# Kernel optimization log

Measured on AMD Instinct MI355X. Metric: run time of the kernel, lower is better.

The kernel has to match this reference:

```python
import jax, jax.numpy as jnp
import numpy as np

NEG = -1e10
EPS = 1e-5
H = 4  # num_heads


def layer_norm(y, g, b):
    m = jnp.mean(y, axis=-1, keepdims=True)
    v = jnp.mean((y - m) ** 2, axis=-1, keepdims=True)
    return (y - m) * jax.lax.rsqrt(v + EPS) * g + b


def setup_inputs() -> dict:
    key = jax.random.key(0)
    B, N, C = 16, 1024, 256
    ks = jax.random.split(key, 12)
    std = 0.1  # matches trunc_normal_(std=0.1) init
    inp = {
        "x": jax.random.normal(ks[0], (B, N, C), jnp.float32),
        "K": jax.random.normal(ks[1], (B, N, N), jnp.float32),
        "n1": jax.random.randint(ks[2], (B,), 8, 33),
        "n2": jax.random.randint(ks[3], (B,), 8, 33),
        "qkv_w": jax.random.normal(ks[4], (3 * C, C), jnp.float32) * std,
        "qkv_b": jnp.zeros((3 * C,), jnp.float32),
        "proj_w": jax.random.normal(ks[5], (C, C), jnp.float32) * std,
        "proj_b": jnp.zeros((C,), jnp.float32),
        "ln1_g": jnp.ones((C,), jnp.float32),
        "ln1_b": jnp.zeros((C,), jnp.float32),
        "ln2_g": jnp.ones((C,), jnp.float32),
        "ln2_b": jnp.zeros((C,), jnp.float32),
        "fc1_w": jax.random.normal(ks[6], (4 * C, C), jnp.float32) * std,
        "fc1_b": jnp.zeros((4 * C,), jnp.float32),
        "fc2_w": jax.random.normal(ks[7], (C, 4 * C), jnp.float32) * std,
        "fc2_b": jnp.zeros((C,), jnp.float32),
    }
    return inp


def reference(x, K, n1, n2, qkv_w, qkv_b, proj_w, proj_b,
              ln1_g, ln1_b, ln2_g, ln2_b, fc1_w, fc1_b, fc2_w, fc2_b):
    B, N, C = x.shape
    D = C // H
    scale = D ** -0.5

    # --- attention block ---
    h = layer_norm(x, ln1_g, ln1_b)
    qkv = (h @ qkv_w.T + qkv_b).reshape(B, N, 3, H, D)
    qkv = jnp.transpose(qkv, (2, 0, 3, 1, 4))  # [3,B,H,N,D]
    q, k, v = qkv[0], qkv[1], qkv[2]

    attn = jnp.einsum('bhnd,bhmd->bhnm', q, k) * scale  # [B,H,N,N]

    # per-sample dynamic block mask: rows>=n1*n2 fully masked; cols>=n1*n2 masked
    nrc = (n1 * n2)[:, None]                  # [B,1]
    invalid = jnp.arange(N)[None, :] >= nrc   # [B,N]
    mask = invalid[:, :, None] | invalid[:, None, :]  # [B,N,N]
    attn = jnp.where(mask[:, None], NEG, attn)
    attn = attn + K[:, None]                  # broadcast K over heads

    a = jax.nn.softmax(attn, axis=-1)
    o = jnp.einsum('bhnm,bhmd->bhnd', a, v)
    o = jnp.transpose(o, (0, 2, 1, 3)).reshape(B, N, C)
    x = x + (o @ proj_w.T + proj_b)

    # --- MLP block (exact GELU as torch nn.GELU) ---
    h2 = layer_norm(x, ln2_g, ln2_b)
    m = jax.nn.gelu(h2 @ fc1_w.T + fc1_b, approximate=False)
    m = m @ fc2_w.T + fc2_b
    return x + m
```

## Files before the change

kernel.cpp:

```cpp
#include <hip/hip_runtime.h>
#include <math.h>
#include <stdint.h>

constexpr int Bc = 16, Nn = 1024, Cc = 256, Hh = 4;
constexpr int Mrows = Bc * Nn;
constexpr float EPSV = 1e-5f;

typedef __attribute__((ext_vector_type(4))) float f32x4;
typedef __attribute__((ext_vector_type(8))) short bf16x8;

__device__ inline float wave_reduce_sum(float v) {
#pragma unroll
  for (int m = 32; m >= 1; m >>= 1) v += __shfl_xor(v, m);
  return v;
}

__device__ inline short f2bf(float f) {
  uint32_t u = __builtin_bit_cast(uint32_t, f);
  u = (u + 0x7fffu + ((u >> 16) & 1u)) >> 16;
  return (short)u;
}
__device__ inline float bf2f(short s) {
  uint32_t u = ((uint32_t)(uint16_t)s) << 16;
  return __builtin_bit_cast(float, u);
}

__device__ inline float fexp(float x) {
  return __builtin_amdgcn_exp2f(x * 1.4426950408889634f);
}

__device__ inline float gelu_fast(float x) {
  float x2 = x * x;
  float u = x * (0.7978845608028654f + 0.0356774081f * x2);
  float e = __builtin_amdgcn_exp2f(u * 2.8853900817779268f);
  return x * (1.f - __builtin_amdgcn_rcpf(e + 1.f));
}

#define GLDS(gptr, lptr)                                             \
  __builtin_amdgcn_global_load_lds(                                  \
      (const __attribute__((address_space(1))) void*)(gptr),         \
      (__attribute__((address_space(3))) void*)(lptr), 16, 0, 0)

__global__ __launch_bounds__(256)
void cvt_bf16(const float* __restrict__ src, short* __restrict__ dst, int n) {
  int i = (blockIdx.x * 256 + threadIdx.x) * 4;
  if (i >= n) return;
  float4 v = *(const float4*)(src + i);
  short4 o;
  o.x = f2bf(v.x); o.y = f2bf(v.y); o.z = f2bf(v.z); o.w = f2bf(v.w);
  *(short4*)(dst + i) = o;
}

__global__ __launch_bounds__(256)
void ln_kernel(const float* __restrict__ x, const float* __restrict__ g,
               const float* __restrict__ b, short* __restrict__ h) {
  int row = blockIdx.x * 4 + (threadIdx.x >> 6);
  int lane = threadIdx.x & 63;
  const float4* xr = (const float4*)(x + (size_t)row * Cc);
  float4 v = xr[lane];
  float s = v.x + v.y + v.z + v.w;
  float sq = v.x * v.x + v.y * v.y + v.z * v.z + v.w * v.w;
  s = wave_reduce_sum(s);
  sq = wave_reduce_sum(sq);
  float mean = s * (1.f / Cc);
  float var = sq * (1.f / Cc) - mean * mean;
  float inv = rsqrtf(var + EPSV);
  float4 gg = ((const float4*)g)[lane];
  float4 bb = ((const float4*)b)[lane];
  short4 o;
  o.x = f2bf((v.x - mean) * inv * gg.x + bb.x);
  o.y = f2bf((v.y - mean) * inv * gg.y + bb.y);
  o.z = f2bf((v.z - mean) * inv * gg.z + bb.z);
  o.w = f2bf((v.w - mean) * inv * gg.w + bb.w);
  *(short4*)(h + (size_t)row * Cc + lane * 4) = o;
}

__global__ __launch_bounds__(256)
void qkv_mfma(const short* __restrict__ A, const short* __restrict__ Bw,
              const float* __restrict__ bias, short* __restrict__ qkp,
              short* __restrict__ vtp) {
  __shared__ __align__(16) short As[128 * 64];
  __shared__ __align__(16) short Bs[128 * 64];
  int t = threadIdx.x;
  int w = t >> 6, lane = t & 63;
  int wm = w >> 1, wn = w & 1;
  int l16 = lane & 15, lhi = lane >> 4;
  int m0 = blockIdx.y * 128, n0 = blockIdx.x * 128;
  const bool vblk = (n0 >= 512);
  f32x4 acc[4][4] = {};

  for (int k0 = 0; k0 < 256; k0 += 64) {
    __syncthreads();
#pragma unroll
    for (int i = 0; i < 4; ++i) {
      int cc = i * 256 + t;
      int r = cc >> 3, sl = cc & 7, ssl = sl ^ (r & 7);
      GLDS(A + (size_t)(m0 + r) * 256 + k0 + ssl * 8, &As[cc * 8]);
      GLDS(Bw + (size_t)(n0 + r) * 256 + k0 + ssl * 8, &Bs[cc * 8]);
    }
    asm volatile("s_waitcnt vmcnt(0)" ::: "memory");
    __syncthreads();
    if (!vblk) {
#pragma unroll
      for (int ks = 0; ks < 2; ++ks) {
        bf16x8 af[4], bg[4];
#pragma unroll
        for (int mi = 0; mi < 4; ++mi) {
          int row = wm * 64 + mi * 16 + l16;
          af[mi] = *(const bf16x8*)&As[row * 64 + ((ks * 32 + lhi * 8) ^ ((row & 7) << 3))];
        }
#pragma unroll
        for (int ni = 0; ni < 4; ++ni) {
          int row = wn * 64 + ni * 16 + l16;
          bg[ni] = *(const bf16x8*)&Bs[row * 64 + ((ks * 32 + lhi * 8) ^ ((row & 7) << 3))];
        }
#pragma unroll
        for (int mi = 0; mi < 4; ++mi)
#pragma unroll
          for (int ni = 0; ni < 4; ++ni)
            acc[mi][ni] = __builtin_amdgcn_mfma_f32_16x16x32_bf16(
                af[mi], bg[ni], acc[mi][ni], 0, 0, 0);
      }
    } else {
#pragma unroll
      for (int ks = 0; ks < 2; ++ks) {
        bf16x8 af[4], bg[4];
#pragma unroll
        for (int mi = 0; mi < 4; ++mi) {
          int row = wm * 64 + mi * 16 + l16;
          af[mi] = *(const bf16x8*)&As[row * 64 + ((ks * 32 + lhi * 8) ^ ((row & 7) << 3))];
        }
#pragma unroll
        for (int ni = 0; ni < 4; ++ni) {
          int row = wn * 64 + ni * 16 + l16;
          bg[ni] = *(const bf16x8*)&Bs[row * 64 + ((ks * 32 + lhi * 8) ^ ((row & 7) << 3))];
        }
#pragma unroll
        for (int mi = 0; mi < 4; ++mi)
#pragma unroll
          for (int ni = 0; ni < 4; ++ni)
            acc[mi][ni] = __builtin_amdgcn_mfma_f32_16x16x32_bf16(
                bg[ni], af[mi], acc[mi][ni], 0, 0, 0);
      }
    }
  }

  if (!vblk) {
    const bool isq = (n0 < 256);
#pragma unroll
    for (int mi = 0; mi < 4; ++mi) {
      int mbase = m0 + wm * 64 + mi * 16 + lhi * 4;
#pragma unroll
      for (int ni = 0; ni < 4; ++ni) {
        int n = n0 + wn * 64 + ni * 16 + l16;
        int s = n >> 8, hh = (n >> 6) & 3, d = n & 63;
        float bv = bias[n];
#pragma unroll
        for (int r = 0; r < 4; ++r) {
          int m = mbase + r;
          int b = m >> 10, rw = m & 1023;
          float v = acc[mi][ni][r] + bv;
          if (isq) v *= 0.125f;
          qkp[(size_t)s * 4194304 + (((size_t)(b * 4 + hh)) * 1024 + rw) * 64 + d] = f2bf(v);
        }
      }
    }
  } else {
#pragma unroll
    for (int mi = 0; mi < 4; ++mi) {
#pragma unroll
      for (int ni = 0; ni < 4; ++ni) {
#pragma unroll
        for (int r = 0; r < 4; ++r) {
          int n = n0 + wn * 64 + ni * 16 + lhi * 4 + r;
          int hh = (n >> 6) & 3, d = n & 63;
          int m = m0 + wm * 64 + mi * 16 + l16;
          int b = m >> 10, rw = m & 1023;
          float v = acc[mi][ni][r] + bias[n];
          vtp[(((size_t)(b * 4 + hh)) * 64 + d) * 1024 + rw] = f2bf(v);
        }
      }
    }
  }
}

__global__ __launch_bounds__(256)
void vmean_kernel(const short* __restrict__ vt, short* __restrict__ vmb) {
  __shared__ float part[64][4];
  int bh = blockIdx.x;
  int d = threadIdx.x >> 2, seg = threadIdx.x & 3;
  const short* p = vt + (size_t)bh * 65536 + (size_t)d * 1024 + seg * 256;
  float s = 0.f;
  for (int i = 0; i < 256; i += 8) {
    bf16x8 v = *(const bf16x8*)(p + i);
#pragma unroll
    for (int j = 0; j < 8; ++j) s += bf2f(v[j]);
  }
  part[d][seg] = s;
  __syncthreads();
  if (threadIdx.x < 64) {
    int dd = threadIdx.x;
    float tot = part[dd][0] + part[dd][1] + part[dd][2] + part[dd][3];
    vmb[bh * 64 + dd] = f2bf(tot * (1.f / 1024.f));
  }
}

__global__ __launch_bounds__(256)
void fattn_mfma(const short* __restrict__ qpk, const short* __restrict__ kpk,
                const short* __restrict__ vt, const float* __restrict__ Kmat,
                const int* __restrict__ n1, const int* __restrict__ n2,
                const short* __restrict__ vmb, short* __restrict__ o) {
  int bh = blockIdx.y, b = bh >> 2, hh = bh & 3;
  int row0 = blockIdx.x * 64;
  int nc = n1[b] * n2[b];
  int t = threadIdx.x;
  __shared__ short vms[64];
  if (t < 64) vms[t] = vmb[bh * 64 + t];
  __syncthreads();
  if (row0 >= nc) {
    for (int idx = t; idx < 4096; idx += 256) {
      int r = idx >> 6, d = idx & 63;
      o[((size_t)(b * 1024 + row0 + r)) * 256 + hh * 64 + d] = vms[d];
    }
    return;
  }
  __shared__ __align__(16) short Ks[2][64 * 64];
  __shared__ __align__(16) short Vs[2][64 * 64];
  __shared__ __align__(16) short Ps[64 * 64];
  int w = t >> 6, lane = t & 63, l16 = lane & 15, lhi = lane >> 4;

  constexpr float LOG2E = 1.4426950408889634f;
  constexpr float MREF = 12.0f;

  const short* qb = qpk + (size_t)bh * 65536 + (size_t)(row0 + w * 16 + l16) * 64;
  bf16x8 qf0 = *(const bf16x8*)(qb + lhi * 8);
  bf16x8 qf1 = *(const bf16x8*)(qb + 32 + lhi * 8);

  f32x4 accO[4] = {};
  float lsum[4] = {};
  const float* Kb = Kmat + (size_t)b * 1048576 + (size_t)(row0 + w * 16) * 1024;

  float kvp[16];

#pragma unroll
  for (int i = 0; i < 2; ++i) {
    int cc = i * 256 + t;
    int r = cc >> 3, sl = cc & 7, ssl = sl ^ (r & 7);
    GLDS(kpk + (size_t)bh * 65536 + (size_t)(0 + r) * 64 + ssl * 8, &Ks[0][cc * 8]);
    GLDS(vt + (size_t)bh * 65536 + (size_t)r * 1024 + 0 + ssl * 8, &Vs[0][cc * 8]);
  }
#pragma unroll
  for (int ni = 0; ni < 4; ++ni)
#pragma unroll
    for (int r = 0; r < 4; ++r)
      kvp[ni * 4 + r] =
          (Kb[(size_t)(lhi * 4 + r) * 1024 + 0 + ni * 16 + l16] - MREF) * LOG2E;

  int cur = 0;
  for (int j0 = 0; j0 < nc; j0 += 64, cur ^= 1) {
    asm volatile("s_waitcnt vmcnt(0)" ::: "memory");
    __syncthreads();

    float kvc[16];
#pragma unroll
    for (int i = 0; i < 16; ++i) kvc[i] = kvp[i];
    int jn = j0 + 64;
    if (jn < nc) {
      int nxt = cur ^ 1;
#pragma unroll
      for (int i = 0; i < 2; ++i) {
        int cc = i * 256 + t;
        int r = cc >> 3, sl = cc & 7, ssl = sl ^ (r & 7);
        GLDS(kpk + (size_t)bh * 65536 + (size_t)(jn + r) * 64 + ssl * 8, &Ks[nxt][cc * 8]);
        GLDS(vt + (size_t)bh * 65536 + (size_t)r * 1024 + jn + ssl * 8, &Vs[nxt][cc * 8]);
      }
#pragma unroll
      for (int ni = 0; ni < 4; ++ni)
#pragma unroll
        for (int r = 0; r < 4; ++r)
          kvp[ni * 4 + r] =
              (Kb[(size_t)(lhi * 4 + r) * 1024 + jn + ni * 16 + l16] - MREF) * LOG2E;
    }

    f32x4 accS[4] = {};
#pragma unroll
    for (int ks = 0; ks < 2; ++ks) {
#pragma unroll
      for (int ni = 0; ni < 4; ++ni) {
        int row = ni * 16 + l16;
        bf16x8 kf = *(const bf16x8*)&Ks[cur][row * 64 + (((ks * 4 + lhi) ^ (row & 7)) << 3)];
        accS[ni] = __builtin_amdgcn_mfma_f32_16x16x32_bf16(
            ks ? qf1 : qf0, kf, accS[ni], 0, 0, 0);
      }
    }

#pragma unroll
    for (int ni = 0; ni < 4; ++ni) {
      bool valid = (j0 + ni * 16 + l16) < nc;
#pragma unroll
      for (int r = 0; r < 4; ++r) {
        float e = __builtin_amdgcn_exp2f(fmaf(accS[ni][r], LOG2E, kvc[ni * 4 + r]));
        e = valid ? e : 0.f;
        lsum[r] += e;
        int prow = w * 16 + lhi * 4 + r;
        int col = ni * 16 + l16;
        Ps[prow * 64 + ((((col >> 3) ^ (prow & 7)) << 3) | (col & 7))] = f2bf(e);
      }
    }

#pragma unroll
    for (int ks = 0; ks < 2; ++ks) {
      int prow = w * 16 + l16;
      bf16x8 pf = *(const bf16x8*)&Ps[prow * 64 + (((ks * 4 + lhi) ^ (prow & 7)) << 3)];
#pragma unroll
      for (int ni = 0; ni < 4; ++ni) {
        int vrow = ni * 16 + l16;
        bf16x8 vf = *(const bf16x8*)&Vs[cur][vrow * 64 + (((ks * 4 + lhi) ^ (vrow & 7)) << 3)];
        accO[ni] = __builtin_amdgcn_mfma_f32_16x16x32_bf16(pf, vf, accO[ni], 0, 0, 0);
      }
    }
  }

#pragma unroll
  for (int r = 0; r < 4; ++r) {
    lsum[r] += __shfl_xor(lsum[r], 1);
    lsum[r] += __shfl_xor(lsum[r], 2);
    lsum[r] += __shfl_xor(lsum[r], 4);
    lsum[r] += __shfl_xor(lsum[r], 8);
  }

#pragma unroll
  for (int ni = 0; ni < 4; ++ni) {
#pragma unroll
    for (int r = 0; r < 4; ++r) {
      int row = row0 + w * 16 + lhi * 4 + r;
      int d = ni * 16 + l16;
      short ov;
      if (row < nc) ov = f2bf(accO[ni][r] * (1.f / lsum[r]));
      else ov = vms[d];
      o[((size_t)(b * 1024 + row)) * 256 + hh * 64 + d] = ov;
    }
  }
}

template <bool GELU, bool RES, bool OUTF, bool OUTB>
__global__ __launch_bounds__(256)
void gemm_mfma(const short* __restrict__ A, const short* __restrict__ Bw,
               const float* __restrict__ bias, const float* __restrict__ resid,
               float* __restrict__ Cf, short* __restrict__ Cb,
               int M, int Nd, int Kd) {
  __shared__ __align__(16) short As[128 * 64];
  __shared__ __align__(16) short Bs[128 * 64];
  int t = threadIdx.x;
  int w = t >> 6, lane = t & 63;
  int wm = w >> 1, wn = w & 1;
  int l16 = lane & 15, lhi = lane >> 4;
  int m0 = blockIdx.y * 128, n0 = blockIdx.x * 128;
  f32x4 acc[4][4] = {};

  for (int k0 = 0; k0 < Kd; k0 += 64) {
    __syncthreads();
#pragma unroll
    for (int i = 0; i < 4; ++i) {
      int cc = i * 256 + t;
      int r = cc >> 3, sl = cc & 7, ssl = sl ^ (r & 7);
      GLDS(A + (size_t)(m0 + r) * Kd + k0 + ssl * 8, &As[cc * 8]);
      GLDS(Bw + (size_t)(n0 + r) * Kd + k0 + ssl * 8, &Bs[cc * 8]);
    }
    asm volatile("s_waitcnt vmcnt(0)" ::: "memory");
    __syncthreads();
#pragma unroll
    for (int ks = 0; ks < 2; ++ks) {
      bf16x8 af[4], bg[4];
#pragma unroll
      for (int mi = 0; mi < 4; ++mi) {
        int row = wm * 64 + mi * 16 + l16;
        af[mi] = *(const bf16x8*)&As[row * 64 + ((ks * 32 + lhi * 8) ^ ((row & 7) << 3))];
      }
#pragma unroll
      for (int ni = 0; ni < 4; ++ni) {
        int row = wn * 64 + ni * 16 + l16;
        bg[ni] = *(const bf16x8*)&Bs[row * 64 + ((ks * 32 + lhi * 8) ^ ((row & 7) << 3))];
      }
#pragma unroll
      for (int mi = 0; mi < 4; ++mi)
#pragma unroll
        for (int ni = 0; ni < 4; ++ni)
          acc[mi][ni] = __builtin_amdgcn_mfma_f32_16x16x32_bf16(
              af[mi], bg[ni], acc[mi][ni], 0, 0, 0);
    }
  }
#pragma unroll
  for (int mi = 0; mi < 4; ++mi) {
    int rbase = m0 + wm * 64 + mi * 16 + lhi * 4;
#pragma unroll
    for (int ni = 0; ni < 4; ++ni) {
      int n = n0 + wn * 64 + ni * 16 + l16;
      float bv = bias[n];
#pragma unroll
      for (int r = 0; r < 4; ++r) {
        int m = rbase + r;
        float v = acc[mi][ni][r] + bv;
        if (GELU) v = gelu_fast(v);
        size_t idx = (size_t)m * Nd + n;
        if (RES) v += resid[idx];
        if (OUTF) Cf[idx] = v;
        if (OUTB) Cb[idx] = f2bf(v);
      }
    }
  }
}

extern "C" void kernel_launch(void* const* d_in, const int* in_sizes, int n_in,
                              void* d_out, int out_size, void* d_ws, size_t ws_size,
                              hipStream_t stream) {
  const float* x      = (const float*)d_in[0];
  const float* Kmat   = (const float*)d_in[1];
  const int*   n1     = (const int*)d_in[2];
  const int*   n2     = (const int*)d_in[3];
  const float* qkv_w  = (const float*)d_in[4];
  const float* qkv_b  = (const float*)d_in[5];
  const float* proj_w = (const float*)d_in[6];
  const float* proj_b = (const float*)d_in[7];
  const float* ln1_g  = (const float*)d_in[8];
  const float* ln1_b  = (const float*)d_in[9];
  const float* ln2_g  = (const float*)d_in[10];
  const float* ln2_b  = (const float*)d_in[11];
  const float* fc1_w  = (const float*)d_in[12];
  const float* fc1_b  = (const float*)d_in[13];
  const float* fc2_w  = (const float*)d_in[14];
  const float* fc2_b  = (const float*)d_in[15];
  float* out = (float*)d_out;

  char* ws = (char*)d_ws;
  constexpr size_t MB = 1024 * 1024;
  short* hb    = (short*)ws;
  short* qkp   = (short*)(ws + 8 * MB);
  short* vtp   = (short*)(ws + 24 * MB);
  short* m1    = (short*)(ws + 8 * MB);
  short* vmb   = (short*)(ws + 40 * MB);
  short* wqkv  = (short*)(ws + 41 * MB);
  short* wproj = (short*)(ws + 42 * MB);
  short* wfc1  = (short*)(ws + 43 * MB);
  short* wfc2  = (short*)(ws + 44 * MB);
  short* obuf  = hb;
  short* qpk   = qkp;
  short* kpk   = qkp + 4194304;

  cvt_bf16<<<dim3(768 * 256 / 1024), 256, 0, stream>>>(qkv_w, wqkv, 768 * 256);
  cvt_bf16<<<dim3(256 * 256 / 1024), 256, 0, stream>>>(proj_w, wproj, 256 * 256);
  cvt_bf16<<<dim3(1024 * 256 / 1024), 256, 0, stream>>>(fc1_w, wfc1, 1024 * 256);
  cvt_bf16<<<dim3(256 * 1024 / 1024), 256, 0, stream>>>(fc2_w, wfc2, 256 * 1024);
  ln_kernel<<<dim3(Mrows / 4), 256, 0, stream>>>(x, ln1_g, ln1_b, hb);
  qkv_mfma<<<dim3(6, 128), 256, 0, stream>>>(hb, wqkv, qkv_b, qkp, vtp);
  vmean_kernel<<<dim3(Bc * Hh), 256, 0, stream>>>(vtp, vmb);
  fattn_mfma<<<dim3(Nn / 64, Bc * Hh), 256, 0, stream>>>(
      qpk, kpk, vtp, Kmat, n1, n2, vmb, obuf);
  gemm_mfma<false, true, true, false><<<dim3(2, 128), 256, 0, stream>>>(
      obuf, wproj, proj_b, x, out, nullptr, Mrows, 256, 256);
  ln_kernel<<<dim3(Mrows / 4), 256, 0, stream>>>(out, ln2_g, ln2_b, hb);
  gemm_mfma<true, false, false, true><<<dim3(8, 128), 256, 0, stream>>>(
      hb, wfc1, fc1_b, nullptr, nullptr, m1, Mrows, 1024, 256);
  gemm_mfma<false, true, true, false><<<dim3(2, 128), 256, 0, stream>>>(
      m1, wfc2, fc2_b, out, out, nullptr, Mrows, 256, 1024);
}
```

Measured before the change: 150.4 us.

## Split KV tiles across waves in attention kernel with 16-row blocks

Each attention block now handles 16 query rows, and its four waves process disjoint KV tiles in parallel, then combine partial outputs and row sums through shared memory. K and V fragments are loaded directly from global memory into registers instead of being double-buffered through LDS. This raises parallelism for the short valid sequence lengths and removes per-tile block barriers. In exchange, K/V global traffic grows through repeated reads across blocks, and there is no software prefetch.

```diff
diff --git a/kernel.cpp b/kernel.cpp
--- a/kernel.cpp
+++ b/kernel.cpp
@@ -23,10 +23,6 @@
 __device__ inline float bf2f(short s) {
   uint32_t u = ((uint32_t)(uint16_t)s) << 16;
   return __builtin_bit_cast(float, u);
-}
-
-__device__ inline float fexp(float x) {
-  return __builtin_amdgcn_exp2f(x * 1.4426950408889634f);
 }
 
 __device__ inline float gelu_fast(float x) {
@@ -211,113 +207,93 @@
                 const int* __restrict__ n1, const int* __restrict__ n2,
                 const short* __restrict__ vmb, short* __restrict__ o) {
   int bh = blockIdx.y, b = bh >> 2, hh = bh & 3;
-  int row0 = blockIdx.x * 64;
+  int row0 = blockIdx.x * 16;
   int nc = n1[b] * n2[b];
   int t = threadIdx.x;
   __shared__ short vms[64];
   if (t < 64) vms[t] = vmb[bh * 64 + t];
   __syncthreads();
   if (row0 >= nc) {
-    for (int idx = t; idx < 4096; idx += 256) {
+    for (int idx = t; idx < 1024; idx += 256) {
       int r = idx >> 6, d = idx & 63;
       o[((size_t)(b * 1024 + row0 + r)) * 256 + hh * 64 + d] = vms[d];
     }
     return;
   }
-  __shared__ __align__(16) short Ks[2][64 * 64];
-  __shared__ __align__(16) short Vs[2][64 * 64];
-  __shared__ __align__(16) short Ps[64 * 64];
+  __shared__ __align__(16) short Ps[4][16 * 64];
+  __shared__ float comb[4][16][65];
+  __shared__ float lsumc[4][16];
+
   int w = t >> 6, lane = t & 63, l16 = lane & 15, lhi = lane >> 4;
 
   constexpr float LOG2E = 1.4426950408889634f;
   constexpr float MREF = 12.0f;
 
-  const short* qb = qpk + (size_t)bh * 65536 + (size_t)(row0 + w * 16 + l16) * 64;
+  const short* qb = qpk + (size_t)bh * 65536 + (size_t)(row0 + l16) * 64;
   bf16x8 qf0 = *(const bf16x8*)(qb + lhi * 8);
   bf16x8 qf1 = *(const bf16x8*)(qb + 32 + lhi * 8);
 
   f32x4 accO[4] = {};
   float lsum[4] = {};
-  const float* Kb = Kmat + (size_t)b * 1048576 + (size_t)(row0 + w * 16) * 1024;
-
-  float kvp[16];
-
-#pragma unroll
-  for (int i = 0; i < 2; ++i) {
-    int cc = i * 256 + t;
-    int r = cc >> 3, sl = cc & 7, ssl = sl ^ (r & 7);
-    GLDS(kpk + (size_t)bh * 65536 + (size_t)(0 + r) * 64 + ssl * 8, &Ks[0][cc * 8]);
-    GLDS(vt + (size_t)bh * 65536 + (size_t)r * 1024 + 0 + ssl * 8, &Vs[0][cc * 8]);
-  }
-#pragma unroll
-  for (int ni = 0; ni < 4; ++ni)
-#pragma unroll
-    for (int r = 0; r < 4; ++r)
-      kvp[ni * 4 + r] =
-          (Kb[(size_t)(lhi * 4 + r) * 1024 + 0 + ni * 16 + l16] - MREF) * LOG2E;
-
-  int cur = 0;
-  for (int j0 = 0; j0 < nc; j0 += 64, cur ^= 1) {
-    asm volatile("s_waitcnt vmcnt(0)" ::: "memory");
-    __syncthreads();
-
-    float kvc[16];
-#pragma unroll
-    for (int i = 0; i < 16; ++i) kvc[i] = kvp[i];
-    int jn = j0 + 64;
-    if (jn < nc) {
-      int nxt = cur ^ 1;
-#pragma unroll
-      for (int i = 0; i < 2; ++i) {
-        int cc = i * 256 + t;
-        int r = cc >> 3, sl = cc & 7, ssl = sl ^ (r & 7);
-        GLDS(kpk + (size_t)bh * 65536 + (size_t)(jn + r) * 64 + ssl * 8, &Ks[nxt][cc * 8]);
-        GLDS(vt + (size_t)bh * 65536 + (size_t)r * 1024 + jn + ssl * 8, &Vs[nxt][cc * 8]);
-      }
+  const float* Kb = Mrows ? Kmat + (size_t)b * 1048576 + (size_t)row0 * 1024 : Kmat;
+  const short* kbase = kpk + (size_t)bh * 65536;
+  const short* vbase = vt + (size_t)bh * 65536;
+  int ntiles = (nc + 63) >> 6;
+
+  for (int jt = w; jt < ntiles; jt += 4) {
+    int j0 = jt * 64;
+    float kv[16];
+#pragma unroll
+    for (int ni = 0; ni < 4; ++ni)
+#pragma unroll
+      for (int r = 0; r < 4; ++r)
+        kv[ni * 4 + r] =
+            (Kb[(size_t)(lhi * 4 + r) * 1024 + j0 + ni * 16 + l16] - MREF) * LOG2E;
+
+    bf16x8 kf[2][4];
+#pragma unroll
+    for (int ks = 0; ks < 2; ++ks)
 #pragma unroll
       for (int ni = 0; ni < 4; ++ni)
-#pragma unroll
-        for (int r = 0; r < 4; ++r)
-          kvp[ni * 4 + r] =
-              (Kb[(size_t)(lhi * 4 + r) * 1024 + jn + ni * 16 + l16] - MREF) * LOG2E;
-    }
+        kf[ks][ni] = *(const bf16x8*)(kbase + (size_t)(j0 + ni * 16 + l16) * 64 +
+                                      ks * 32 + lhi * 8);
+    bf16x8 vf[2][4];
+#pragma unroll
+    for (int ks = 0; ks < 2; ++ks)
+#pragma unroll
+      for (int ni = 0; ni < 4; ++ni)
+        vf[ks][ni] = *(const bf16x8*)(vbase + (size_t)(ni * 16 + l16) * 1024 + j0 +
+                                      ks * 32 + lhi * 8);
 
     f32x4 accS[4] = {};
 #pragma unroll
-    for (int ks = 0; ks < 2; ++ks) {
-#pragma unroll
-      for (int ni = 0; ni < 4; ++ni) {
-        int row = ni * 16 + l16;
-        bf16x8 kf = *(const bf16x8*)&Ks[cur][row * 64 + (((ks * 4 + lhi) ^ (row & 7)) << 3)];
+    for (int ks = 0; ks < 2; ++ks)
+#pragma unroll
+      for (int ni = 0; ni < 4; ++ni)
         accS[ni] = __builtin_amdgcn_mfma_f32_16x16x32_bf16(
-            ks ? qf1 : qf0, kf, accS[ni], 0, 0, 0);
-      }
-    }
+            ks ? qf1 : qf0, kf[ks][ni], accS[ni], 0, 0, 0);
 
 #pragma unroll
     for (int ni = 0; ni < 4; ++ni) {
       bool valid = (j0 + ni * 16 + l16) < nc;
 #pragma unroll
       for (int r = 0; r < 4; ++r) {
-        float e = __builtin_amdgcn_exp2f(fmaf(accS[ni][r], LOG2E, kvc[ni * 4 + r]));
+        float e = __builtin_amdgcn_exp2f(fmaf(accS[ni][r], LOG2E, kv[ni * 4 + r]));
         e = valid ? e : 0.f;
         lsum[r] += e;
-        int prow = w * 16 + lhi * 4 + r;
+        int prow = lhi * 4 + r;
         int col = ni * 16 + l16;
-        Ps[prow * 64 + ((((col >> 3) ^ (prow & 7)) << 3) | (col & 7))] = f2bf(e);
+        Ps[w][prow * 64 + ((((col >> 3) ^ (prow & 7)) << 3) | (col & 7))] = f2bf(e);
       }
     }
 
 #pragma unroll
     for (int ks = 0; ks < 2; ++ks) {
-      int prow = w * 16 + l16;
-      bf16x8 pf = *(const bf16x8*)&Ps[prow * 64 + (((ks * 4 + lhi) ^ (prow & 7)) << 3)];
-#pragma unroll
-      for (int ni = 0; ni < 4; ++ni) {
-        int vrow = ni * 16 + l16;
-        bf16x8 vf = *(const bf16x8*)&Vs[cur][vrow * 64 + (((ks * 4 + lhi) ^ (vrow & 7)) << 3)];
-        accO[ni] = __builtin_amdgcn_mfma_f32_16x16x32_bf16(pf, vf, accO[ni], 0, 0, 0);
-      }
+      bf16x8 pf = *(const bf16x8*)&Ps[w][l16 * 64 + (((ks * 4 + lhi) ^ (l16 & 7)) << 3)];
+#pragma unroll
+      for (int ni = 0; ni < 4; ++ni)
+        accO[ni] = __builtin_amdgcn_mfma_f32_16x16x32_bf16(pf, vf[ks][ni], accO[ni],
+                                                           0, 0, 0);
     }
   }
 
@@ -330,16 +306,28 @@
   }
 
 #pragma unroll
-  for (int ni = 0; ni < 4; ++ni) {
-#pragma unroll
-    for (int r = 0; r < 4; ++r) {
-      int row = row0 + w * 16 + lhi * 4 + r;
-      int d = ni * 16 + l16;
-      short ov;
-      if (row < nc) ov = f2bf(accO[ni][r] * (1.f / lsum[r]));
-      else ov = vms[d];
-      o[((size_t)(b * 1024 + row)) * 256 + hh * 64 + d] = ov;
-    }
+  for (int ni = 0; ni < 4; ++ni)
+#pragma unroll
+    for (int r = 0; r < 4; ++r)
+      comb[w][lhi * 4 + r][ni * 16 + l16] = accO[ni][r];
+  if (l16 == 0) {
+#pragma unroll
+    for (int r = 0; r < 4; ++r) lsumc[w][lhi * 4 + r] = lsum[r];
+  }
+  __syncthreads();
+
+  for (int idx = t; idx < 1024; idx += 256) {
+    int q = idx >> 6, d = idx & 63;
+    int row = row0 + q;
+    short ov;
+    if (row < nc) {
+      float s = comb[0][q][d] + comb[1][q][d] + comb[2][q][d] + comb[3][q][d];
+      float L = lsumc[0][q] + lsumc[1][q] + lsumc[2][q] + lsumc[3][q];
+      ov = f2bf(s * (1.f / L));
+    } else {
+      ov = vms[d];
+    }
+    o[((size_t)(b * 1024 + row)) * 256 + hh * 64 + d] = ov;
   }
 }
 
@@ -454,7 +442,7 @@
   ln_kernel<<<dim3(Mrows / 4), 256, 0, stream>>>(x, ln1_g, ln1_b, hb);
   qkv_mfma<<<dim3(6, 128), 256, 0, stream>>>(hb, wqkv, qkv_b, qkp, vtp);
   vmean_kernel<<<dim3(Bc * Hh), 256, 0, stream>>>(vtp, vmb);
-  fattn_mfma<<<dim3(Nn / 64, Bc * Hh), 256, 0, stream>>>(
+  fattn_mfma<<<dim3(Nn / 16, Bc * Hh), 256, 0, stream>>>(
       qpk, kpk, vtp, Kmat, n1, n2, vmb, obuf);
   gemm_mfma<false, true, true, false><<<dim3(2, 128), 256, 0, stream>>>(
       obuf, wproj, proj_b, x, out, nullptr, Mrows, 256, 256);
```

Result: slower. 164.7 us (+9.5%).
